# Kernel optimization log

Hardware: AMD Instinct MI355X
Metric: run time of the kernel (lower is better)

## Reference

```python
import jax, jax.numpy as jnp
import numpy as np
import math

NUM_HEADS = 16
HIDDEN = 1024
MLP = 4096
SEQ = 2048
HEAD_DIM = HIDDEN // NUM_HEADS  # 64
EPS = 1e-5


def setup_inputs() -> dict:
    key = jax.random.key(0)
    ks = jax.random.split(key, 16)
    s = 0.02
    inp = {
        "x": jax.random.normal(ks[0], (SEQ, HIDDEN), jnp.float32),
        "rope_cos": jnp.cos(jnp.arange(SEQ, dtype=jnp.float32)[:, None] * (1.0 / (10000.0 ** (jnp.arange(HEAD_DIM // 2, dtype=jnp.float32) * 2 / HEAD_DIM)))[None, :]),
        "rope_sin": jnp.sin(jnp.arange(SEQ, dtype=jnp.float32)[:, None] * (1.0 / (10000.0 ** (jnp.arange(HEAD_DIM // 2, dtype=jnp.float32) * 2 / HEAD_DIM)))[None, :]),
        "norm0_w": jnp.ones((HIDDEN,), jnp.float32),
        "norm0_b": jnp.zeros((HIDDEN,), jnp.float32),
        "norm1_w": jnp.ones((HIDDEN,), jnp.float32),
        "norm1_b": jnp.zeros((HIDDEN,), jnp.float32),
        "wqkv_w": jax.random.normal(ks[1], (3 * HIDDEN, HIDDEN), jnp.float32) * s,
        "wqkv_b": jnp.zeros((3 * HIDDEN,), jnp.float32),
        "wo_w": jax.random.normal(ks[2], (HIDDEN, HIDDEN), jnp.float32) * s,
        "wo_b": jnp.zeros((HIDDEN,), jnp.float32),
        "up_w": jax.random.normal(ks[3], (MLP, HIDDEN), jnp.float32) * s,
        "up_b": jnp.zeros((MLP,), jnp.float32),
        "down_w": jax.random.normal(ks[4], (HIDDEN, MLP), jnp.float32) * s,
        "down_b": jnp.zeros((HIDDEN,), jnp.float32),
        # 4 packed sequences of length 512 each
        "input_row_offsets": jnp.array([0, 512, 1024, 1536, 2048], jnp.int32),
    }
    return inp


def _layernorm(x, w, b):
    m = jnp.mean(x, axis=-1, keepdims=True)
    v = jnp.mean((x - m) ** 2, axis=-1, keepdims=True)
    return (x - m) * jax.lax.rsqrt(v + EPS) * w + b


def _rope(t, cos, sin):
    # t: [S, nh, hd]; cos/sin: [S, hd/2] -> complex rotation of adjacent pairs
    S, nh, hd = t.shape
    t2 = t.reshape(S, nh, hd // 2, 2)
    re, im = t2[..., 0], t2[..., 1]
    c = cos[:, None, :]
    s = sin[:, None, :]
    out = jnp.stack([re * c - im * s, re * s + im * c], axis=-1)
    return out.reshape(S, nh, hd)


def _block(x, rope_cos, rope_sin, norm0_w, norm0_b, wqkv_w, wqkv_b, wo_w, wo_b,
           up_w, up_b, down_w, down_b, norm1_w, norm1_b, input_row_offsets):
    S, H = x.shape
    nh, hd = NUM_HEADS, HEAD_DIM
    h = _layernorm(x, norm0_w, norm0_b)
    qkv = (h @ wqkv_w.T + wqkv_b).reshape(S, 3, nh, hd)
    q, k, v = qkv[:, 0], qkv[:, 1], qkv[:, 2]
    q = _rope(q, rope_cos, rope_sin)
    k = _rope(k, rope_cos, rope_sin)
    # block-diagonal bool mask added as 0/1 float (matches torch `attn_weight += bool_mask`)
    seg = jnp.searchsorted(input_row_offsets, jnp.arange(S), side="right") - 1
    mask = (seg[:, None] == seg[None, :]).astype(jnp.float32)  # [S, S]
    scores = jnp.einsum("shd,thd->hst", q, k) / math.sqrt(hd) + mask[None]
    attn = jax.nn.softmax(scores.astype(jnp.float32), axis=-1).astype(q.dtype)
    out = jnp.einsum("hst,thd->shd", attn, v).reshape(S, H)
    x = x + (out @ wo_w.T + wo_b)
    h = _layernorm(x, norm1_w, norm1_b)
    h = jax.nn.gelu(h @ up_w.T + up_b, approximate=True)
    return x + (h @ down_w.T + down_b)


def reference(x, rope_cos, rope_sin, norm0_w, norm0_b, norm1_w, norm1_b,
              wqkv_w, wqkv_b, wo_w, wo_b, up_w, up_b, down_w, down_b,
              input_row_offsets):
    return _block(x, rope_cos, rope_sin, norm0_w, norm0_b, wqkv_w, wqkv_b,
                  wo_w, wo_b, up_w, up_b, down_w, down_b, norm1_w, norm1_b,
                  input_row_offsets)
```

## Files before the change

### kernel.cpp

```cpp
#include <hip/hip_runtime.h>
#include <hip/hip_bf16.h>
#include <math.h>

#define SEQ 2048
#define HID 1024
#define NH 16
#define HD 64

using f32x4  = __attribute__((ext_vector_type(4))) float;
using bf16x8 = __attribute__((ext_vector_type(8))) short;

union U8 { unsigned int u[4]; bf16x8 v; short s[8]; };

__device__ __forceinline__ short f2bf(float f) {
  unsigned int x = __float_as_uint(f);
  unsigned int r = (x + 0x7fffu + ((x >> 16) & 1u)) >> 16;
  return (short)(r & 0xffffu);
}

__device__ __forceinline__ unsigned int pkbf(float a, float b) {
  return ((unsigned int)(unsigned short)f2bf(a)) |
         (((unsigned int)(unsigned short)f2bf(b)) << 16);
}

__device__ __forceinline__ float bf2f_lo(unsigned int u) {
  return __uint_as_float((u & 0xffffu) << 16);
}
__device__ __forceinline__ float bf2f_hi(unsigned int u) {
  return __uint_as_float(u & 0xffff0000u);
}

__device__ __forceinline__ float fast_exp2(float x) {
#if __has_builtin(__builtin_amdgcn_exp2f)
  return __builtin_amdgcn_exp2f(x);
#else
  return exp2f(x);
#endif
}

__device__ __forceinline__ float fast_rcp(float x) {
#if __has_builtin(__builtin_amdgcn_rcpf)
  return __builtin_amdgcn_rcpf(x);
#else
  return 1.0f / x;
#endif
}

__device__ __forceinline__ void async_cp16(const void* g, void* l) {
  __builtin_amdgcn_global_load_lds(
      (__attribute__((address_space(1))) void*)(g),
      (__attribute__((address_space(3))) void*)(l), 16, 0, 0);
}

__global__ void cvt_all_kernel(const float* __restrict__ a, const float* __restrict__ b,
                               const float* __restrict__ c, const float* __restrict__ d,
                               short* __restrict__ oa, short* __restrict__ ob,
                               short* __restrict__ oc, short* __restrict__ od) {
  int i = blockIdx.x * blockDim.x + threadIdx.x;
  const float* src; short* dst; int off;
  if (i < 786432)        { src = a; dst = oa; off = i; }
  else if (i < 1048576)  { src = b; dst = ob; off = i - 786432; }
  else if (i < 2097152)  { src = c; dst = oc; off = i - 1048576; }
  else                   { src = d; dst = od; off = i - 2097152; }
  float4 v = ((const float4*)src)[off];
  short4 o;
  o.x = f2bf(v.x); o.y = f2bf(v.y); o.z = f2bf(v.z); o.w = f2bf(v.w);
  ((short4*)dst)[off] = o;
}

__global__ __launch_bounds__(256) void ln_kernel(const float* __restrict__ x,
    const float* __restrict__ w, const float* __restrict__ b, short* __restrict__ out) {
  int row = blockIdx.x;
  int tid = threadIdx.x;
  float4 v = ((const float4*)(x + (size_t)row * HID))[tid];
  float s  = v.x + v.y + v.z + v.w;
  float s2 = v.x*v.x + v.y*v.y + v.z*v.z + v.w*v.w;
#pragma unroll
  for (int o = 32; o >= 1; o >>= 1) {
    s  += __shfl_xor(s,  o);
    s2 += __shfl_xor(s2, o);
  }
  __shared__ float red[8];
  int wv = tid >> 6;
  if ((tid & 63) == 0) { red[wv] = s; red[4 + wv] = s2; }
  __syncthreads();
  float ts  = red[0] + red[1] + red[2] + red[3];
  float ts2 = red[4] + red[5] + red[6] + red[7];
  float mean = ts * (1.0f / HID);
  float var  = ts2 * (1.0f / HID) - mean * mean;
  float rs = rsqrtf(var + 1e-5f);
  float4 wv4 = ((const float4*)w)[tid];
  float4 bv4 = ((const float4*)b)[tid];
  short4 o;
  o.x = f2bf((v.x - mean) * rs * wv4.x + bv4.x);
  o.y = f2bf((v.y - mean) * rs * wv4.y + bv4.y);
  o.z = f2bf((v.z - mean) * rs * wv4.z + bv4.z);
  o.w = f2bf((v.w - mean) * rs * wv4.w + bv4.w);
  ((short4*)(out + (size_t)row * HID))[tid] = o;
}

__global__ void rope_qk_kernel(const short* __restrict__ qkvb,
    const float* __restrict__ cosb, const float* __restrict__ sinb,
    short* __restrict__ Qh, short* __restrict__ Kh) {
  int tid = blockIdx.x * blockDim.x + threadIdx.x;
  int s   = tid >> 10;
  int r   = tid & 1023;
  int j   = r >> 9;
  int rem = r & 511;
  int h   = rem >> 5;
  int i   = rem & 31;
  int d   = i * 2;
  unsigned int u = *(const unsigned int*)(qkvb + (size_t)s * 3072 + j * 1024 + h * 64 + d);
  float a = bf2f_lo(u), b = bf2f_hi(u);
  float c  = cosb[s * 32 + i];
  float sn = sinb[s * 32 + i];
  float scale = (j == 0) ? 0.18033688011112043f : 1.0f;
  unsigned int o = pkbf(scale * (a * c - b * sn), scale * (a * sn + b * c));
  short* dst = (j == 0 ? Qh : Kh) + ((size_t)h * SEQ + s) * HD + d;
  *(unsigned int*)dst = o;
}

__global__ __launch_bounds__(256) void vtrans_kernel(const short* __restrict__ qkvb,
                                                     short* __restrict__ Vt) {
  __shared__ short tile[64 * 72];
  int s0   = blockIdx.x * 64;
  int head = blockIdx.y;
  int tid  = threadIdx.x;
#pragma unroll
  for (int p = 0; p < 2; p++) {
    int seg = p * 256 + tid;
    int row = seg >> 3;
    int c8  = seg & 7;
    bf16x8 v = *(const bf16x8*)(qkvb + (size_t)(s0 + row) * 3072 + 2048 + head * 64 + c8 * 8);
    *(bf16x8*)(tile + row * 72 + c8 * 8) = v;
  }
  __syncthreads();
#pragma unroll
  for (int p = 0; p < 2; p++) {
    int seg = p * 256 + tid;
    int d   = seg >> 3;
    int sc  = seg & 7;
    U8 o;
#pragma unroll
    for (int j = 0; j < 8; j++) o.s[j] = tile[(sc * 8 + j) * 72 + d];
    *(bf16x8*)(Vt + ((size_t)head * HD + d) * SEQ + s0 + sc * 8) = o.v;
  }
}

template <int EPI>
__global__ __launch_bounds__(256) void gemm_bt_kernel(
    const short* __restrict__ A, const short* __restrict__ B,
    const float* __restrict__ bias, const float* __restrict__ resid,
    void* __restrict__ outp, int M, int N, int Klen, int Kstride) {
  __shared__ __attribute__((aligned(16))) short Alds[128 * 32];
  __shared__ __attribute__((aligned(16))) short Blds[128 * 32];
  int tid = threadIdx.x;
  int w    = tid >> 6;
  int lane = tid & 63;
  int lcol  = lane & 15;
  int lhalf = lane >> 4;
  int m0 = blockIdx.y * 128;
  int n0 = blockIdx.x * 128;
  int z  = blockIdx.z;
  int wm = (w & 1) * 64;
  int wn = (w >> 1) * 64;

  const short* apt[2];
  const short* bpt[2];
#pragma unroll
  for (int p = 0; p < 2; p++) {
    int seg = p * 256 + tid;
    int row = seg >> 2;
    int c   = (seg & 3) ^ ((row >> 1) & 3);
    apt[p] = A + (size_t)z * Klen + (size_t)(m0 + row) * Kstride + c * 8;
    bpt[p] = B + (size_t)z * Klen + (size_t)(n0 + row) * Kstride + c * 8;
  }
  int sw = (lhalf ^ ((lcol >> 1) & 3)) * 8;

  f32x4 acc[4][4];
#pragma unroll
  for (int i = 0; i < 4; i++)
#pragma unroll
    for (int j = 0; j < 4; j++) acc[i][j] = (f32x4){0.f, 0.f, 0.f, 0.f};

  for (int k0 = 0; k0 < Klen; k0 += 32) {
#pragma unroll
    for (int p = 0; p < 2; p++) {
      async_cp16(apt[p], Alds + p * 2048 + w * 512);  apt[p] += 32;
      async_cp16(bpt[p], Blds + p * 2048 + w * 512);  bpt[p] += 32;
    }
    __syncthreads();
    bf16x8 af[4], bfr[4];
#pragma unroll
    for (int i = 0; i < 4; i++)
      af[i] = *(const bf16x8*)(Alds + (wm + i * 16 + lcol) * 32 + sw);
#pragma unroll
    for (int j = 0; j < 4; j++)
      bfr[j] = *(const bf16x8*)(Blds + (wn + j * 16 + lcol) * 32 + sw);
#pragma unroll
    for (int i = 0; i < 4; i++)
#pragma unroll
      for (int j = 0; j < 4; j++)
        acc[i][j] = __builtin_amdgcn_mfma_f32_16x16x32_bf16(af[i], bfr[j], acc[i][j], 0, 0, 0);
    __syncthreads();
  }

#pragma unroll
  for (int i = 0; i < 4; i++) {
#pragma unroll
    for (int j = 0; j < 4; j++) {
#pragma unroll
      for (int r = 0; r < 4; r++) {
        int row = m0 + wm + i * 16 + lhalf * 4 + r;
        int col = n0 + wn + j * 16 + lcol;
        float v = acc[i][j][r];
        if (EPI != 5) v += bias[col];
        if (EPI == 2) {
          float t = v * (1.5957691216057308f + 0.07135481283942279f * v * v);
          float e = fast_exp2(t * -1.4426950408889634f);
          v = v * fast_rcp(1.0f + e);
          ((short*)outp)[(size_t)row * N + col] = f2bf(v);
        } else if (EPI == 3) {
          ((short*)outp)[(size_t)row * N + col] = f2bf(v);
        } else {
          ((short*)outp)[(size_t)z * M * N + (size_t)row * N + col] = f2bf(v);
        }
      }
    }
  }
}

__global__ __launch_bounds__(256) void attn_kernel(
    const short* __restrict__ Qh, const short* __restrict__ Kh,
    const short* __restrict__ Vt, const int* __restrict__ offs,
    short* __restrict__ Opart, float* __restrict__ Lpart) {
  __shared__ __attribute__((aligned(16))) short Klds[64 * 64];
  __shared__ __attribute__((aligned(16))) short Vlds[64 * 64];
  __shared__ __attribute__((aligned(16))) unsigned int Plds[4][16 * 34];
  int head = blockIdx.y;
  int q0   = blockIdx.x * 64;
  int z    = blockIdx.z;
  int tid  = threadIdx.x;
  int w    = tid >> 6;
  int lane = tid & 63;
  int lcol = lane & 15;
  int h    = lane >> 4;
  int s7   = lcol & 7;
  int o1 = offs[1], o2 = offs[2], o3 = offs[3];

  int qrow = q0 + w * 16 + lcol;
  const short* qb = Qh + ((size_t)head * SEQ + qrow) * HD;
  bf16x8 qf0 = *(const bf16x8*)(qb + h * 8);
  bf16x8 qf1 = *(const bf16x8*)(qb + 32 + h * 8);
  int sq = (qrow >= o1) + (qrow >= o2) + (qrow >= o3);
  U8 qe;
  qe.u[0] = 0; qe.u[1] = 0; qe.u[2] = 0; qe.u[3] = 0;
  if (h == 0) qe.s[sq] = (short)0x3FB9;

  bf16x8 ones;
#pragma unroll
  for (int i = 0; i < 8; i++) ones[i] = 0x3F80;

  int kb0 = lcol * 64 + ((h ^ s7) * 8);
  int kb1 = lcol * 64 + (((4 + h) ^ s7) * 8);
  int vb0 = lcol * 64 + ((h ^ s7) * 8);
  int vb1 = lcol * 64 + (((4 + h) ^ s7) * 8);
  int pwb = lcol * 34 + h * 2;
  int prb = lcol * 34 + h * 4;

  int tbeg = z * 512;
  const short* kp0; const short* kp1; const short* vp0; const short* vp1;
  {
    int seg = tid, row = seg >> 3, g = (seg & 7) ^ (row & 7);
    kp0 = Kh + ((size_t)head * SEQ + tbeg + row) * HD + g * 8;
    vp0 = Vt + ((size_t)head * HD + row) * SEQ + tbeg + g * 8;
    seg = 256 + tid; row = seg >> 3; g = (seg & 7) ^ (row & 7);
    kp1 = Kh + ((size_t)head * SEQ + tbeg + row) * HD + g * 8;
    vp1 = Vt + ((size_t)head * HD + row) * SEQ + tbeg + g * 8;
  }

  f32x4 o_acc[4];
#pragma unroll
  for (int nt = 0; nt < 4; nt++) o_acc[nt] = (f32x4){0.f, 0.f, 0.f, 0.f};
  f32x4 acc_l = (f32x4){0.f, 0.f, 0.f, 0.f};

  for (int t0 = 0; t0 < 512; t0 += 64) {
    async_cp16(kp0, Klds + w * 512);          kp0 += 64 * HD;
    async_cp16(kp1, Klds + 2048 + w * 512);   kp1 += 64 * HD;
    async_cp16(vp0, Vlds + w * 512);          vp0 += 64;
    async_cp16(vp1, Vlds + 2048 + w * 512);   vp1 += 64;
    __syncthreads();

#pragma unroll
    for (int n = 0; n < 4; n++) {
      bf16x8 kf0 = *(const bf16x8*)(Klds + n * 1024 + kb0);
      bf16x8 kf1 = *(const bf16x8*)(Klds + n * 1024 + kb1);
      int key = tbeg + t0 + n * 16 + lcol;
      int sk = (key >= o1) + (key >= o2) + (key >= o3);
      U8 ke;
      ke.u[0] = (h == 0) ? ((sk == 0) ? 0x00003F80u : (sk == 1) ? 0x3F800000u : 0u) : 0u;
      ke.u[1] = (h == 0) ? ((sk == 2) ? 0x00003F80u : (sk == 3) ? 0x3F800000u : 0u) : 0u;
      ke.u[2] = 0; ke.u[3] = 0;

      f32x4 sacc = (f32x4){0.f, 0.f, 0.f, 0.f};
      sacc = __builtin_amdgcn_mfma_f32_16x16x32_bf16(kf0, qf0, sacc, 0, 0, 0);
      sacc = __builtin_amdgcn_mfma_f32_16x16x32_bf16(kf1, qf1, sacc, 0, 0, 0);
      sacc = __builtin_amdgcn_mfma_f32_16x16x32_bf16(ke.v, qe.v, sacc, 0, 0, 0);

      float p0 = fast_exp2(sacc[0]);
      float p1 = fast_exp2(sacc[1]);
      float p2 = fast_exp2(sacc[2]);
      float p3 = fast_exp2(sacc[3]);
      uint2 pw;
      pw.x = __builtin_amdgcn_perm(__float_as_uint(p1), __float_as_uint(p0), 0x07060302);
      pw.y = __builtin_amdgcn_perm(__float_as_uint(p3), __float_as_uint(p2), 0x07060302);
      *(uint2*)&Plds[w][pwb + n * 8] = pw;
    }

#pragma unroll
    for (int kc = 0; kc < 2; kc++) {
      uint2 a = *(const uint2*)&Plds[w][prb + kc * 16];
      uint2 b = *(const uint2*)&Plds[w][prb + kc * 16 + 2];
      U8 pu;
      pu.u[0] = a.x; pu.u[1] = a.y; pu.u[2] = b.x; pu.u[3] = b.y;
      int vb = kc ? vb1 : vb0;
#pragma unroll
      for (int nt = 0; nt < 4; nt++) {
        bf16x8 vf = *(const bf16x8*)(Vlds + nt * 1024 + vb);
        o_acc[nt] = __builtin_amdgcn_mfma_f32_16x16x32_bf16(vf, pu.v, o_acc[nt], 0, 0, 0);
      }
      acc_l = __builtin_amdgcn_mfma_f32_16x16x32_bf16(ones, pu.v, acc_l, 0, 0, 0);
    }
    __syncthreads();
  }

  short* op = Opart + ((size_t)z * SEQ + qrow) * HID + head * HD + h * 4;
#pragma unroll
  for (int nt = 0; nt < 4; nt++) {
    uint2 ua;
    ua.x = pkbf(o_acc[nt][0], o_acc[nt][1]);
    ua.y = pkbf(o_acc[nt][2], o_acc[nt][3]);
    *(uint2*)(op + nt * 16) = ua;
  }
  if (lane < 16)
    Lpart[((size_t)z * NH + head) * SEQ + qrow] = acc_l[0];
}

__global__ __launch_bounds__(256) void attn_merge_kernel(
    const short* __restrict__ Opart, const float* __restrict__ Lpart,
    short* __restrict__ attn) {
  int i = blockIdx.x * blockDim.x + threadIdx.x;
  int col4 = i & 255;
  int row  = i >> 8;
  int head = col4 >> 4;
  float acc0 = 0.f, acc1 = 0.f, acc2 = 0.f, acc3 = 0.f, l = 0.f;
#pragma unroll
  for (int zz = 0; zz < 4; zz++) {
    uint2 p = ((const uint2*)(Opart + (size_t)zz * SEQ * HID))[i];
    acc0 += bf2f_lo(p.x); acc1 += bf2f_hi(p.x);
    acc2 += bf2f_lo(p.y); acc3 += bf2f_hi(p.y);
    l += Lpart[((size_t)zz * NH + head) * SEQ + row];
  }
  float rl = fast_rcp(l);
  uint2 o;
  o.x = pkbf(acc0 * rl, acc1 * rl);
  o.y = pkbf(acc2 * rl, acc3 * rl);
  ((uint2*)attn)[i] = o;
}

__global__ __launch_bounds__(256) void merge_ln_kernel(
    const short* __restrict__ part, const float* __restrict__ bias,
    const float* __restrict__ resid, const float* __restrict__ w,
    const float* __restrict__ b, float* __restrict__ x1, short* __restrict__ h1) {
  int row = blockIdx.x;
  int tid = threadIdx.x;
  size_t idx = (size_t)row * HID / 4 + tid;
  float4 v = {0.f, 0.f, 0.f, 0.f};
#pragma unroll
  for (int z = 0; z < 4; z++) {
    uint2 p = ((const uint2*)(part + (size_t)z * SEQ * HID))[idx];
    v.x += bf2f_lo(p.x); v.y += bf2f_hi(p.x);
    v.z += bf2f_lo(p.y); v.w += bf2f_hi(p.y);
  }
  float4 bi = ((const float4*)bias)[tid];
  float4 rs4 = ((const float4*)(resid + (size_t)row * HID))[tid];
  v.x += bi.x + rs4.x; v.y += bi.y + rs4.y; v.z += bi.z + rs4.z; v.w += bi.w + rs4.w;
  ((float4*)(x1 + (size_t)row * HID))[tid] = v;
  float s  = v.x + v.y + v.z + v.w;
  float s2 = v.x*v.x + v.y*v.y + v.z*v.z + v.w*v.w;
#pragma unroll
  for (int o = 32; o >= 1; o >>= 1) {
    s  += __shfl_xor(s,  o);
    s2 += __shfl_xor(s2, o);
  }
  __shared__ float red[8];
  int wv = tid >> 6;
  if ((tid & 63) == 0) { red[wv] = s; red[4 + wv] = s2; }
  __syncthreads();
  float ts  = red[0] + red[1] + red[2] + red[3];
  float ts2 = red[4] + red[5] + red[6] + red[7];
  float mean = ts * (1.0f / HID);
  float var  = ts2 * (1.0f / HID) - mean * mean;
  float rsq = rsqrtf(var + 1e-5f);
  float4 wv4 = ((const float4*)w)[tid];
  float4 bv4 = ((const float4*)b)[tid];
  short4 o;
  o.x = f2bf((v.x - mean) * rsq * wv4.x + bv4.x);
  o.y = f2bf((v.y - mean) * rsq * wv4.y + bv4.y);
  o.z = f2bf((v.z - mean) * rsq * wv4.z + bv4.z);
  o.w = f2bf((v.w - mean) * rsq * wv4.w + bv4.w);
  ((short4*)(h1 + (size_t)row * HID))[tid] = o;
}

__global__ __launch_bounds__(256) void merge_bias_kernel(
    const short* __restrict__ part, const float* __restrict__ bias,
    const float* __restrict__ resid, float* __restrict__ out) {
  int i = blockIdx.x * blockDim.x + threadIdx.x;
  int col4 = i & 255;
  float4 v = {0.f, 0.f, 0.f, 0.f};
#pragma unroll
  for (int z = 0; z < 4; z++) {
    uint2 p = ((const uint2*)(part + (size_t)z * SEQ * HID))[i];
    v.x += bf2f_lo(p.x); v.y += bf2f_hi(p.x);
    v.z += bf2f_lo(p.y); v.w += bf2f_hi(p.y);
  }
  float4 bi = ((const float4*)bias)[col4];
  float4 rs = ((const float4*)resid)[i];
  float4 o;
  o.x = v.x + bi.x + rs.x;
  o.y = v.y + bi.y + rs.y;
  o.z = v.z + bi.z + rs.z;
  o.w = v.w + bi.w + rs.w;
  ((float4*)out)[i] = o;
}

extern "C" void kernel_launch(void* const* d_in, const int* in_sizes, int n_in,
                              void* d_out, int out_size, void* d_ws, size_t ws_size,
                              hipStream_t stream) {
  const float* x      = (const float*)d_in[0];
  const float* ropec  = (const float*)d_in[1];
  const float* ropes  = (const float*)d_in[2];
  const float* n0w    = (const float*)d_in[3];
  const float* n0b    = (const float*)d_in[4];
  const float* n1w    = (const float*)d_in[5];
  const float* n1b    = (const float*)d_in[6];
  const float* wqkv_w = (const float*)d_in[7];
  const float* wqkv_b = (const float*)d_in[8];
  const float* wo_w   = (const float*)d_in[9];
  const float* wo_b   = (const float*)d_in[10];
  const float* up_w   = (const float*)d_in[11];
  const float* up_b   = (const float*)d_in[12];
  const float* down_w = (const float*)d_in[13];
  const float* down_b = (const float*)d_in[14];
  const int*   offs   = (const int*)d_in[15];
  float* out = (float*)d_out;

  char* base = (char*)d_ws;
  short* wqkv_bf = (short*)(base + 0);
  short* wo_bf   = (short*)(base + 6291456);
  short* up_bf   = (short*)(base + 8388608);
  short* down_bf = (short*)(base + 16777216);
  short* h0      = (short*)(base + 25165824);
  short* qkv_bf  = (short*)(base + 29360128);
  short* Qh      = (short*)(base + 41943040);
  short* Kh      = (short*)(base + 46137344);
  short* Vt      = (short*)(base + 50331648);
  short* Opart   = (short*)(base + 54525952);
  float* Lpart   = (float*)(base + 71303168);
  short* attn    = (short*)(base + 71827456);
  float* x1      = (float*)(base + 76021760);
  short* h1      = (short*)(base + 84410368);
  short* wopart  = (short*)(base + 25165824);
  short* u       = (short*)(base + 25165824);
  short* dnpart  = (short*)(base + 41943040);

  cvt_all_kernel<<<12288, 256, 0, stream>>>(wqkv_w, wo_w, up_w, down_w,
                                            wqkv_bf, wo_bf, up_bf, down_bf);
  ln_kernel<<<2048, 256, 0, stream>>>(x, n0w, n0b, h0);
  gemm_bt_kernel<3><<<dim3(24, 16), 256, 0, stream>>>(h0, wqkv_bf, wqkv_b, nullptr,
                                                      qkv_bf, 2048, 3072, 1024, 1024);
  rope_qk_kernel<<<8192, 256, 0, stream>>>(qkv_bf, ropec, ropes, Qh, Kh);
  vtrans_kernel<<<dim3(32, 16), 256, 0, stream>>>(qkv_bf, Vt);
  attn_kernel<<<dim3(32, 16, 4), 256, 0, stream>>>(Qh, Kh, Vt, offs, Opart, Lpart);
  attn_merge_kernel<<<2048, 256, 0, stream>>>(Opart, Lpart, attn);
  gemm_bt_kernel<5><<<dim3(8, 16, 4), 256, 0, stream>>>(attn, wo_bf, nullptr, nullptr,
                                                        wopart, 2048, 1024, 256, 1024);
  merge_ln_kernel<<<2048, 256, 0, stream>>>(wopart, wo_b, x, n1w, n1b, x1, h1);
  gemm_bt_kernel<2><<<dim3(32, 16), 256, 0, stream>>>(h1, up_bf, up_b, nullptr,
                                                      u, 2048, 4096, 1024, 1024);
  gemm_bt_kernel<5><<<dim3(8, 16, 4), 256, 0, stream>>>(u, down_bf, nullptr, nullptr,
                                                        dnpart, 2048, 1024, 1024, 4096);
  merge_bias_kernel<<<2048, 256, 0, stream>>>(dnpart, down_b, x1, out);
}
```

Baseline: 290.2 us.

## Split-K all GEMMs and move bias/GELU/residual into generic merge kernel

Every GEMM now uses split-K and writes bf16 partial sums: the QKV and up projections are split in two, and the down projection goes from four splits to eight. A templated merge kernel then sums the partials and applies bias, GELU or residual in place of the in-GEMM epilogues. The aim is more workgroups on the 256-CU device for the GEMMs that had few tiles. The cost is extra launches, extra partial-buffer traffic, and an added bf16 rounding of each partial.

```diff
diff --git a/kernel.cpp b/kernel.cpp
--- a/kernel.cpp
+++ b/kernel.cpp
@@ -44,6 +44,12 @@
 #else
   return 1.0f / x;
 #endif
+}
+
+__device__ __forceinline__ float gelu_t(float v) {
+  float t = v * (1.5957691216057308f + 0.07135481283942279f * v * v);
+  float e = fast_exp2(t * -1.4426950408889634f);
+  return v * fast_rcp(1.0f + e);
 }
 
 __device__ __forceinline__ void async_cp16(const void* g, void* l) {
@@ -150,7 +156,6 @@
 template <int EPI>
 __global__ __launch_bounds__(256) void gemm_bt_kernel(
     const short* __restrict__ A, const short* __restrict__ B,
-    const float* __restrict__ bias, const float* __restrict__ resid,
     void* __restrict__ outp, int M, int N, int Klen, int Kstride) {
   __shared__ __attribute__((aligned(16))) short Alds[128 * 32];
   __shared__ __attribute__((aligned(16))) short Blds[128 * 32];
@@ -213,20 +218,41 @@
       for (int r = 0; r < 4; r++) {
         int row = m0 + wm + i * 16 + lhalf * 4 + r;
         int col = n0 + wn + j * 16 + lcol;
-        float v = acc[i][j][r];
-        if (EPI != 5) v += bias[col];
-        if (EPI == 2) {
-          float t = v * (1.5957691216057308f + 0.07135481283942279f * v * v);
-          float e = fast_exp2(t * -1.4426950408889634f);
-          v = v * fast_rcp(1.0f + e);
-          ((short*)outp)[(size_t)row * N + col] = f2bf(v);
-        } else if (EPI == 3) {
-          ((short*)outp)[(size_t)row * N + col] = f2bf(v);
-        } else {
-          ((short*)outp)[(size_t)z * M * N + (size_t)row * N + col] = f2bf(v);
-        }
+        ((short*)outp)[(size_t)z * M * N + (size_t)row * N + col] = f2bf(acc[i][j][r]);
       }
     }
+  }
+}
+
+template <int NZ, int EPI>
+__global__ __launch_bounds__(256) void merge_k(
+    const short* __restrict__ part, const float* __restrict__ bias,
+    const float* __restrict__ resid, void* __restrict__ outp, int N4) {
+  int row = blockIdx.y;
+  int c4  = blockIdx.x * 256 + threadIdx.x;
+  size_t i = (size_t)row * N4 + c4;
+  size_t MN4 = (size_t)gridDim.y * N4;
+  float4 v = {0.f, 0.f, 0.f, 0.f};
+#pragma unroll
+  for (int z = 0; z < NZ; z++) {
+    uint2 p = ((const uint2*)part)[z * MN4 + i];
+    v.x += bf2f_lo(p.x); v.y += bf2f_hi(p.x);
+    v.z += bf2f_lo(p.y); v.w += bf2f_hi(p.y);
+  }
+  float4 bi = ((const float4*)bias)[c4];
+  v.x += bi.x; v.y += bi.y; v.z += bi.z; v.w += bi.w;
+  if (EPI == 1) {
+    v.x = gelu_t(v.x); v.y = gelu_t(v.y); v.z = gelu_t(v.z); v.w = gelu_t(v.w);
+  }
+  if (EPI == 2) {
+    float4 rs = ((const float4*)resid)[i];
+    v.x += rs.x; v.y += rs.y; v.z += rs.z; v.w += rs.w;
+    ((float4*)outp)[i] = v;
+  } else {
+    uint2 o;
+    o.x = pkbf(v.x, v.y);
+    o.y = pkbf(v.z, v.w);
+    ((uint2*)outp)[i] = o;
   }
 }
 
@@ -263,8 +289,7 @@
 
   int kb0 = lcol * 64 + ((h ^ s7) * 8);
   int kb1 = lcol * 64 + (((4 + h) ^ s7) * 8);
-  int vb0 = lcol * 64 + ((h ^ s7) * 8);
-  int vb1 = lcol * 64 + (((4 + h) ^ s7) * 8);
+  int vb0 = kb0, vb1 = kb1;
   int pwb = lcol * 34 + h * 2;
   int prb = lcol * 34 + h * 4;
 
@@ -410,28 +435,6 @@
   o.z = f2bf((v.z - mean) * rsq * wv4.z + bv4.z);
   o.w = f2bf((v.w - mean) * rsq * wv4.w + bv4.w);
   ((short4*)(h1 + (size_t)row * HID))[tid] = o;
-}
-
-__global__ __launch_bounds__(256) void merge_bias_kernel(
-    const short* __restrict__ part, const float* __restrict__ bias,
-    const float* __restrict__ resid, float* __restrict__ out) {
-  int i = blockIdx.x * blockDim.x + threadIdx.x;
-  int col4 = i & 255;
-  float4 v = {0.f, 0.f, 0.f, 0.f};
-#pragma unroll
-  for (int z = 0; z < 4; z++) {
-    uint2 p = ((const uint2*)(part + (size_t)z * SEQ * HID))[i];
-    v.x += bf2f_lo(p.x); v.y += bf2f_hi(p.x);
-    v.z += bf2f_lo(p.y); v.w += bf2f_hi(p.y);
-  }
-  float4 bi = ((const float4*)bias)[col4];
-  float4 rs = ((const float4*)resid)[i];
-  float4 o;
-  o.x = v.x + bi.x + rs.x;
-  o.y = v.y + bi.y + rs.y;
-  o.z = v.z + bi.z + rs.z;
-  o.w = v.w + bi.w + rs.w;
-  ((float4*)out)[i] = o;
 }
 
 extern "C" void kernel_launch(void* const* d_in, const int* in_sizes, int n_in,
@@ -470,25 +473,29 @@
   short* attn    = (short*)(base + 71827456);
   float* x1      = (float*)(base + 76021760);
   short* h1      = (short*)(base + 84410368);
+  short* qkvpart = (short*)(base + 41943040);
   short* wopart  = (short*)(base + 25165824);
-  short* u       = (short*)(base + 25165824);
-  short* dnpart  = (short*)(base + 41943040);
+  short* uppart  = (short*)(base + 25165824);
+  short* u       = (short*)(base + 58720256);
+  short* dnpart  = (short*)(base + 25165824);
 
   cvt_all_kernel<<<12288, 256, 0, stream>>>(wqkv_w, wo_w, up_w, down_w,
                                             wqkv_bf, wo_bf, up_bf, down_bf);
   ln_kernel<<<2048, 256, 0, stream>>>(x, n0w, n0b, h0);
-  gemm_bt_kernel<3><<<dim3(24, 16), 256, 0, stream>>>(h0, wqkv_bf, wqkv_b, nullptr,
-                                                      qkv_bf, 2048, 3072, 1024, 1024);
+  gemm_bt_kernel<5><<<dim3(24, 16, 2), 256, 0, stream>>>(h0, wqkv_bf, qkvpart,
+                                                         2048, 3072, 512, 1024);
+  merge_k<2, 0><<<dim3(3, 2048), 256, 0, stream>>>(qkvpart, wqkv_b, nullptr, qkv_bf, 768);
   rope_qk_kernel<<<8192, 256, 0, stream>>>(qkv_bf, ropec, ropes, Qh, Kh);
   vtrans_kernel<<<dim3(32, 16), 256, 0, stream>>>(qkv_bf, Vt);
   attn_kernel<<<dim3(32, 16, 4), 256, 0, stream>>>(Qh, Kh, Vt, offs, Opart, Lpart);
   attn_merge_kernel<<<2048, 256, 0, stream>>>(Opart, Lpart, attn);
-  gemm_bt_kernel<5><<<dim3(8, 16, 4), 256, 0, stream>>>(attn, wo_bf, nullptr, nullptr,
-                                                        wopart, 2048, 1024, 256, 1024);
+  gemm_bt_kernel<5><<<dim3(8, 16, 4), 256, 0, stream>>>(attn, wo_bf, wopart,
+                                                        2048, 1024, 256, 1024);
   merge_ln_kernel<<<2048, 256, 0, stream>>>(wopart, wo_b, x, n1w, n1b, x1, h1);
-  gemm_bt_kernel<2><<<dim3(32, 16), 256, 0, stream>>>(h1, up_bf, up_b, nullptr,
-                                                      u, 2048, 4096, 1024, 1024);
-  gemm_bt_kernel<5><<<dim3(8, 16, 4), 256, 0, stream>>>(u, down_bf, nullptr, nullptr,
-                                                        dnpart, 2048, 1024, 1024, 4096);
-  merge_bias_kernel<<<2048, 256, 0, stream>>>(dnpart, down_b, x1, out);
-}
+  gemm_bt_kernel<5><<<dim3(32, 16, 2), 256, 0, stream>>>(h1, up_bf, uppart,
+                                                         2048, 4096, 512, 1024);
+  merge_k<2, 1><<<dim3(4, 2048), 256, 0, stream>>>(uppart, up_b, nullptr, u, 1024);
+  gemm_bt_kernel<5><<<dim3(8, 16, 8), 256, 0, stream>>>(u, down_bf, dnpart,
+                                                        2048, 1024, 512, 4096);
+  merge_k<8, 2><<<dim3(1, 2048), 256, 0, stream>>>(dnpart, down_b, x1, out, 256);
+}
```

After: 313.8 us. 1.08x slower.

## Rework attention kernel to 32x32 MFMA tiles with register-prefetched K/V

Applied to the files above, without the earlier changes.

Each attention block now handles 128 query rows (32 per wave) and uses 32x32x16 bf16 MFMAs instead of 16x16x32 for both QK^T and PV. K/V tiles are staged through registers with a one-tile-ahead prefetch into padded (stride 72) LDS, replacing async copies into XOR-swizzled LDS. The softmax denominator is summed in registers with a lane shuffle instead of an extra MFMA against a ones vector. The grid is halved along the query dimension. The aim is more reuse per K/V tile and fewer MFMA issues, at the cost of more registers and lower occupancy.

```diff
diff --git a/kernel.cpp b/kernel.cpp
--- a/kernel.cpp
+++ b/kernel.cpp
@@ -7,8 +7,9 @@
 #define NH 16
 #define HD 64
 
-using f32x4  = __attribute__((ext_vector_type(4))) float;
-using bf16x8 = __attribute__((ext_vector_type(8))) short;
+using f32x4   = __attribute__((ext_vector_type(4))) float;
+using f32x16  = __attribute__((ext_vector_type(16))) float;
+using bf16x8  = __attribute__((ext_vector_type(8))) short;
 
 union U8 { unsigned int u[4]; bf16x8 v; short s[8]; };
 
@@ -234,116 +235,129 @@
     const short* __restrict__ Qh, const short* __restrict__ Kh,
     const short* __restrict__ Vt, const int* __restrict__ offs,
     short* __restrict__ Opart, float* __restrict__ Lpart) {
-  __shared__ __attribute__((aligned(16))) short Klds[64 * 64];
-  __shared__ __attribute__((aligned(16))) short Vlds[64 * 64];
-  __shared__ __attribute__((aligned(16))) unsigned int Plds[4][16 * 34];
+  __shared__ __attribute__((aligned(16))) short Klds[64 * 72];
+  __shared__ __attribute__((aligned(16))) short Vlds[64 * 72];
+  __shared__ __attribute__((aligned(16))) short Plds[4][32 * 72];
   int head = blockIdx.y;
-  int q0   = blockIdx.x * 64;
+  int q0   = blockIdx.x * 128;
   int z    = blockIdx.z;
   int tid  = threadIdx.x;
   int w    = tid >> 6;
   int lane = tid & 63;
-  int lcol = lane & 15;
-  int h    = lane >> 4;
-  int s7   = lcol & 7;
+  int l31  = lane & 31;
+  int lh   = lane >> 5;
   int o1 = offs[1], o2 = offs[2], o3 = offs[3];
 
-  int qrow = q0 + w * 16 + lcol;
-  const short* qb = Qh + ((size_t)head * SEQ + qrow) * HD;
-  bf16x8 qf0 = *(const bf16x8*)(qb + h * 8);
-  bf16x8 qf1 = *(const bf16x8*)(qb + 32 + h * 8);
+  int qrow = q0 + w * 32 + l31;
+  const short* qb = Qh + ((size_t)head * SEQ + qrow) * HD + lh * 8;
+  bf16x8 qf0 = *(const bf16x8*)(qb);
+  bf16x8 qf1 = *(const bf16x8*)(qb + 16);
+  bf16x8 qf2 = *(const bf16x8*)(qb + 32);
+  bf16x8 qf3 = *(const bf16x8*)(qb + 48);
   int sq = (qrow >= o1) + (qrow >= o2) + (qrow >= o3);
   U8 qe;
   qe.u[0] = 0; qe.u[1] = 0; qe.u[2] = 0; qe.u[3] = 0;
-  if (h == 0) qe.s[sq] = (short)0x3FB9;
-
-  bf16x8 ones;
-#pragma unroll
-  for (int i = 0; i < 8; i++) ones[i] = 0x3F80;
-
-  int kb0 = lcol * 64 + ((h ^ s7) * 8);
-  int kb1 = lcol * 64 + (((4 + h) ^ s7) * 8);
-  int vb0 = lcol * 64 + ((h ^ s7) * 8);
-  int vb1 = lcol * 64 + (((4 + h) ^ s7) * 8);
-  int pwb = lcol * 34 + h * 2;
-  int prb = lcol * 34 + h * 4;
-
+  if (lh == 0) qe.s[sq] = (short)0x3FB9;
+
+  int srow = tid >> 3;
+  int sc   = tid & 7;
   int tbeg = z * 512;
-  const short* kp0; const short* kp1; const short* vp0; const short* vp1;
-  {
-    int seg = tid, row = seg >> 3, g = (seg & 7) ^ (row & 7);
-    kp0 = Kh + ((size_t)head * SEQ + tbeg + row) * HD + g * 8;
-    vp0 = Vt + ((size_t)head * HD + row) * SEQ + tbeg + g * 8;
-    seg = 256 + tid; row = seg >> 3; g = (seg & 7) ^ (row & 7);
-    kp1 = Kh + ((size_t)head * SEQ + tbeg + row) * HD + g * 8;
-    vp1 = Vt + ((size_t)head * HD + row) * SEQ + tbeg + g * 8;
-  }
-
-  f32x4 o_acc[4];
-#pragma unroll
-  for (int nt = 0; nt < 4; nt++) o_acc[nt] = (f32x4){0.f, 0.f, 0.f, 0.f};
-  f32x4 acc_l = (f32x4){0.f, 0.f, 0.f, 0.f};
+  const short* kg0 = Kh + ((size_t)head * SEQ + tbeg + srow) * HD + sc * 8;
+  const short* kg1 = kg0 + (size_t)32 * HD;
+  const short* vg0 = Vt + ((size_t)head * HD + srow) * SEQ + tbeg + sc * 8;
+  const short* vg1 = vg0 + (size_t)32 * SEQ;
+  short* kw0 = Klds + srow * 72 + sc * 8;
+  short* kw1 = kw0 + 32 * 72;
+  short* vw0 = Vlds + srow * 72 + sc * 8;
+  short* vw1 = vw0 + 32 * 72;
+
+  bf16x8 rk0 = *(const bf16x8*)kg0;  kg0 += (size_t)64 * HD;
+  bf16x8 rk1 = *(const bf16x8*)kg1;  kg1 += (size_t)64 * HD;
+  bf16x8 rv0 = *(const bf16x8*)vg0;  vg0 += 64;
+  bf16x8 rv1 = *(const bf16x8*)vg1;  vg1 += 64;
+
+  f32x16 oA, oB;
+#pragma unroll
+  for (int i = 0; i < 16; i++) { oA[i] = 0.f; oB[i] = 0.f; }
+  float l_lane = 0.f;
+
+  short* prow = Plds[w] + l31 * 72;
+  const short* ka_base = Klds + l31 * 72 + lh * 8;
+  const short* va_base = Vlds + l31 * 72 + lh * 8;
+  const short* pb_base = prow + lh * 8;
 
   for (int t0 = 0; t0 < 512; t0 += 64) {
-    async_cp16(kp0, Klds + w * 512);          kp0 += 64 * HD;
-    async_cp16(kp1, Klds + 2048 + w * 512);   kp1 += 64 * HD;
-    async_cp16(vp0, Vlds + w * 512);          vp0 += 64;
-    async_cp16(vp1, Vlds + 2048 + w * 512);   vp1 += 64;
     __syncthreads();
-
-#pragma unroll
-    for (int n = 0; n < 4; n++) {
-      bf16x8 kf0 = *(const bf16x8*)(Klds + n * 1024 + kb0);
-      bf16x8 kf1 = *(const bf16x8*)(Klds + n * 1024 + kb1);
-      int key = tbeg + t0 + n * 16 + lcol;
+    *(bf16x8*)kw0 = rk0;
+    *(bf16x8*)kw1 = rk1;
+    *(bf16x8*)vw0 = rv0;
+    *(bf16x8*)vw1 = rv1;
+    if (t0 + 64 < 512) {
+      rk0 = *(const bf16x8*)kg0;  kg0 += (size_t)64 * HD;
+      rk1 = *(const bf16x8*)kg1;  kg1 += (size_t)64 * HD;
+      rv0 = *(const bf16x8*)vg0;  vg0 += 64;
+      rv1 = *(const bf16x8*)vg1;  vg1 += 64;
+    }
+    __syncthreads();
+
+#pragma unroll
+    for (int kt = 0; kt < 2; kt++) {
+      int key = tbeg + t0 + kt * 32 + l31;
       int sk = (key >= o1) + (key >= o2) + (key >= o3);
       U8 ke;
-      ke.u[0] = (h == 0) ? ((sk == 0) ? 0x00003F80u : (sk == 1) ? 0x3F800000u : 0u) : 0u;
-      ke.u[1] = (h == 0) ? ((sk == 2) ? 0x00003F80u : (sk == 3) ? 0x3F800000u : 0u) : 0u;
-      ke.u[2] = 0; ke.u[3] = 0;
-
-      f32x4 sacc = (f32x4){0.f, 0.f, 0.f, 0.f};
-      sacc = __builtin_amdgcn_mfma_f32_16x16x32_bf16(kf0, qf0, sacc, 0, 0, 0);
-      sacc = __builtin_amdgcn_mfma_f32_16x16x32_bf16(kf1, qf1, sacc, 0, 0, 0);
-      sacc = __builtin_amdgcn_mfma_f32_16x16x32_bf16(ke.v, qe.v, sacc, 0, 0, 0);
-
-      float p0 = fast_exp2(sacc[0]);
-      float p1 = fast_exp2(sacc[1]);
-      float p2 = fast_exp2(sacc[2]);
-      float p3 = fast_exp2(sacc[3]);
-      uint2 pw;
-      pw.x = __builtin_amdgcn_perm(__float_as_uint(p1), __float_as_uint(p0), 0x07060302);
-      pw.y = __builtin_amdgcn_perm(__float_as_uint(p3), __float_as_uint(p2), 0x07060302);
-      *(uint2*)&Plds[w][pwb + n * 8] = pw;
+      ke.u[0] = 0; ke.u[1] = 0; ke.u[2] = 0; ke.u[3] = 0;
+      if (lh == 0) ke.s[sk] = (short)0x3F80;
+
+      const short* ka = ka_base + kt * (32 * 72);
+      f32x16 s;
+#pragma unroll
+      for (int i = 0; i < 16; i++) s[i] = 0.f;
+      s = __builtin_amdgcn_mfma_f32_32x32x16_bf16(*(const bf16x8*)(ka),      qf0, s, 0, 0, 0);
+      s = __builtin_amdgcn_mfma_f32_32x32x16_bf16(*(const bf16x8*)(ka + 16), qf1, s, 0, 0, 0);
+      s = __builtin_amdgcn_mfma_f32_32x32x16_bf16(*(const bf16x8*)(ka + 32), qf2, s, 0, 0, 0);
+      s = __builtin_amdgcn_mfma_f32_32x32x16_bf16(*(const bf16x8*)(ka + 48), qf3, s, 0, 0, 0);
+      s = __builtin_amdgcn_mfma_f32_32x32x16_bf16(ke.v, qe.v, s, 0, 0, 0);
+
+      float e[16];
+#pragma unroll
+      for (int i = 0; i < 16; i++) e[i] = fast_exp2(s[i]);
+#pragma unroll
+      for (int i = 0; i < 16; i++) l_lane += e[i];
+#pragma unroll
+      for (int g = 0; g < 4; g++) {
+        uint2 pw;
+        pw.x = __builtin_amdgcn_perm(__float_as_uint(e[4 * g + 1]),
+                                     __float_as_uint(e[4 * g + 0]), 0x07060302);
+        pw.y = __builtin_amdgcn_perm(__float_as_uint(e[4 * g + 3]),
+                                     __float_as_uint(e[4 * g + 2]), 0x07060302);
+        *(uint2*)(prow + kt * 32 + g * 8 + lh * 4) = pw;
+      }
     }
 
 #pragma unroll
-    for (int kc = 0; kc < 2; kc++) {
-      uint2 a = *(const uint2*)&Plds[w][prb + kc * 16];
-      uint2 b = *(const uint2*)&Plds[w][prb + kc * 16 + 2];
-      U8 pu;
-      pu.u[0] = a.x; pu.u[1] = a.y; pu.u[2] = b.x; pu.u[3] = b.y;
-      int vb = kc ? vb1 : vb0;
-#pragma unroll
-      for (int nt = 0; nt < 4; nt++) {
-        bf16x8 vf = *(const bf16x8*)(Vlds + nt * 1024 + vb);
-        o_acc[nt] = __builtin_amdgcn_mfma_f32_16x16x32_bf16(vf, pu.v, o_acc[nt], 0, 0, 0);
-      }
-      acc_l = __builtin_amdgcn_mfma_f32_16x16x32_bf16(ones, pu.v, acc_l, 0, 0, 0);
+    for (int kc = 0; kc < 4; kc++) {
+      bf16x8 pf = *(const bf16x8*)(pb_base + kc * 16);
+      bf16x8 va = *(const bf16x8*)(va_base + kc * 16);
+      bf16x8 vb = *(const bf16x8*)(va_base + 32 * 72 + kc * 16);
+      oA = __builtin_amdgcn_mfma_f32_32x32x16_bf16(va, pf, oA, 0, 0, 0);
+      oB = __builtin_amdgcn_mfma_f32_32x32x16_bf16(vb, pf, oB, 0, 0, 0);
     }
-    __syncthreads();
-  }
-
-  short* op = Opart + ((size_t)z * SEQ + qrow) * HID + head * HD + h * 4;
-#pragma unroll
-  for (int nt = 0; nt < 4; nt++) {
-    uint2 ua;
-    ua.x = pkbf(o_acc[nt][0], o_acc[nt][1]);
-    ua.y = pkbf(o_acc[nt][2], o_acc[nt][3]);
-    *(uint2*)(op + nt * 16) = ua;
-  }
-  if (lane < 16)
-    Lpart[((size_t)z * NH + head) * SEQ + qrow] = acc_l[0];
+  }
+
+  float lsum = l_lane + __shfl_xor(l_lane, 32);
+  short* op = Opart + ((size_t)z * SEQ + qrow) * HID + head * HD + lh * 4;
+#pragma unroll
+  for (int g = 0; g < 4; g++) {
+    uint2 ua, ub;
+    ua.x = pkbf(oA[4 * g + 0], oA[4 * g + 1]);
+    ua.y = pkbf(oA[4 * g + 2], oA[4 * g + 3]);
+    ub.x = pkbf(oB[4 * g + 0], oB[4 * g + 1]);
+    ub.y = pkbf(oB[4 * g + 2], oB[4 * g + 3]);
+    *(uint2*)(op + g * 8) = ua;
+    *(uint2*)(op + 32 + g * 8) = ub;
+  }
+  if (lh == 0)
+    Lpart[((size_t)z * NH + head) * SEQ + qrow] = lsum;
 }
 
 __global__ __launch_bounds__(256) void attn_merge_kernel(
@@ -481,7 +495,7 @@
                                                       qkv_bf, 2048, 3072, 1024, 1024);
   rope_qk_kernel<<<8192, 256, 0, stream>>>(qkv_bf, ropec, ropes, Qh, Kh);
   vtrans_kernel<<<dim3(32, 16), 256, 0, stream>>>(qkv_bf, Vt);
-  attn_kernel<<<dim3(32, 16, 4), 256, 0, stream>>>(Qh, Kh, Vt, offs, Opart, Lpart);
+  attn_kernel<<<dim3(16, 16, 4), 256, 0, stream>>>(Qh, Kh, Vt, offs, Opart, Lpart);
   attn_merge_kernel<<<2048, 256, 0, stream>>>(Opart, Lpart, attn);
   gemm_bt_kernel<5><<<dim3(8, 16, 4), 256, 0, stream>>>(attn, wo_bf, nullptr, nullptr,
                                                         wopart, 2048, 1024, 256, 1024);
```

Result: slower. 329.6 us (+13.6%).
